# Kernel optimization log

Hardware: AMD Instinct MI355X
Metric: run time of the kernel (lower is better)

## Reference

```python
import jax, jax.numpy as jnp
import numpy as np

B, S, E, H = 2, 2048, 1024, 16
DK = E // H  # 64


def setup_inputs() -> dict:
    key = jax.random.key(0)
    ks = jax.random.split(key, 5)
    scale = 1.0 / np.sqrt(E)
    return {
        "x": jax.random.normal(ks[0], (B, S, E), dtype=jnp.float32),
        "Wq": jax.random.normal(ks[1], (E, E), dtype=jnp.float32) * scale,
        "Wk": jax.random.normal(ks[2], (E, E), dtype=jnp.float32) * scale,
        "Wv": jax.random.normal(ks[3], (E, E), dtype=jnp.float32) * scale,
        "Wo": jax.random.normal(ks[4], (E, E), dtype=jnp.float32) * scale,
    }


def reference(x, Wq, Wk, Wv, Wo):
    # Linear layers: y = x @ W.T (torch nn.Linear convention, bias=False)
    b, s, e = x.shape
    q = (x @ Wq.T).reshape(b, s, H, DK)  # (B,S,H,dk)
    k = (x @ Wk.T).reshape(b, s, H, DK)
    v = (x @ Wv.T).reshape(b, s, H, DK)
    # scores = Q K^T / sqrt(d_k)  -> (B,H,Sq,Sk)
    scores = jnp.einsum("bihd,bkhd->bhik", q, k) / jnp.sqrt(jnp.asarray(DK, x.dtype))
    p = jax.nn.softmax(scores, axis=-1)
    # dropout is identity in eval/deterministic mode
    attn = jnp.einsum("bhik,bkhd->bihd", p, v)  # (B,S,H,dk)
    concat = attn.reshape(b, s, e)
    return concat @ Wo.T
```

## Files before the change

### kernel.cpp

```cpp
#include <hip/hip_runtime.h>
#include <hip/hip_bf16.h>
#include <cstdint>
#include <cstddef>

typedef __bf16 bf16_t;
typedef __attribute__((ext_vector_type(8))) __bf16 bf16x8;
typedef __attribute__((ext_vector_type(4))) __bf16 bf16x4;
typedef __attribute__((ext_vector_type(4))) float f32x4;
typedef __attribute__((ext_vector_type(16))) float f32x16;
typedef uint32_t u32;
typedef __attribute__((ext_vector_type(4))) u32 u32x4;
typedef __attribute__((ext_vector_type(2))) u32 u32x2;

constexpr int B_ = 2, S_ = 2048, E_ = 1024, H_ = 16, DK_ = 64;

__device__ __forceinline__ void gl2lds16(const void* g, void* l) {
  __builtin_amdgcn_global_load_lds(
      (const __attribute__((address_space(1))) void*)g,
      (__attribute__((address_space(3))) void*)l, 16, 0, 0);
}

__device__ __forceinline__ float exp2_(float x) {
#if __has_builtin(__builtin_amdgcn_exp2f)
  return __builtin_amdgcn_exp2f(x);
#else
  return exp2f(x);
#endif
}

__device__ __forceinline__ u32 cvtpk(float lo, float hi) {
  u32 r;
  asm("v_cvt_pk_bf16_f32 %0, %1, %2" : "=v"(r) : "v"(lo), "v"(hi));
  return r;
}

__device__ __forceinline__ void pl32swap(u32& a, u32& b) {
#if __has_builtin(__builtin_amdgcn_permlane32_swap)
  const u32x2 r = __builtin_amdgcn_permlane32_swap(a, b, false, false);
  a = r[0]; b = r[1];
#else
  asm volatile("v_permlane32_swap_b32 %0, %1" : "+v"(a), "+v"(b));
#endif
}

__device__ __forceinline__ bf16x8 ldsfrag(const char* base, int row, int chunk) {
  return *reinterpret_cast<const bf16x8*>(base + row * 128 + (((chunk ^ (row & 7))) << 4));
}

__global__ __launch_bounds__(256) void f2bf_kernel(const float* __restrict__ in,
                                                   bf16_t* __restrict__ out, int n4) {
  int i = blockIdx.x * 256 + threadIdx.x;
  if (i >= n4) return;
  const float4 v = reinterpret_cast<const float4*>(in)[i];
  bf16x4 o;
  o[0] = (bf16_t)v.x; o[1] = (bf16_t)v.y; o[2] = (bf16_t)v.z; o[3] = (bf16_t)v.w;
  reinterpret_cast<bf16x4*>(out)[i] = o;
}

__global__ __launch_bounds__(256) void f2bf_w(const float* __restrict__ w0,
                                              const float* __restrict__ w1,
                                              const float* __restrict__ w2,
                                              const float* __restrict__ w3,
                                              bf16_t* __restrict__ out) {
  const int i = blockIdx.x * 256 + threadIdx.x;
  const int seg = i >> 18, off = i & 262143;
  const float* src = seg == 0 ? w0 : seg == 1 ? w1 : seg == 2 ? w2 : w3;
  const float4 v = reinterpret_cast<const float4*>(src)[off];
  bf16x4 o;
  o[0] = (bf16_t)v.x; o[1] = (bf16_t)v.y; o[2] = (bf16_t)v.z; o[3] = (bf16_t)v.w;
  reinterpret_cast<bf16x4*>(out)[i] = o;
}

__global__ __launch_bounds__(256) void gemm_qkv(const bf16_t* __restrict__ A,
                                                const bf16_t* __restrict__ Bt,
                                                bf16_t* __restrict__ Qo,
                                                bf16_t* __restrict__ Ko,
                                                bf16_t* __restrict__ Vto,
                                                int K, float qscale) {
  __shared__ bf16_t As[128 * 32];
  __shared__ bf16_t Bs[128 * 32];
  const int tid = threadIdx.x;
  const int w = tid >> 6, l = tid & 63;
  const int wr = w >> 1, wc = w & 1;
  const int tm = blockIdx.x * 128, tn = blockIdx.y * 128;
  f32x4 acc[4][4] = {};

  for (int k0 = 0; k0 < K; k0 += 32) {
#pragma unroll
    for (int i = 0; i < 2; ++i) {
      const int r = i * 64 + w * 16 + (l >> 2);
      const int c = k0 + (l & 3) * 8;
      gl2lds16(A + (size_t)(tm + r) * K + c, As + (i * 64 + w * 16) * 32);
      gl2lds16(Bt + (size_t)(tn + r) * K + c, Bs + (i * 64 + w * 16) * 32);
    }
    __syncthreads();

    bf16x8 af[4], bfr[4];
#pragma unroll
    for (int mi = 0; mi < 4; ++mi)
      af[mi] = *reinterpret_cast<const bf16x8*>(
          As + (wr * 64 + mi * 16 + (l & 15)) * 32 + (l >> 4) * 8);
#pragma unroll
    for (int ni = 0; ni < 4; ++ni)
      bfr[ni] = *reinterpret_cast<const bf16x8*>(
          Bs + (wc * 64 + ni * 16 + (l & 15)) * 32 + (l >> 4) * 8);
#pragma unroll
    for (int mi = 0; mi < 4; ++mi)
#pragma unroll
      for (int ni = 0; ni < 4; ++ni)
        acc[mi][ni] =
            __builtin_amdgcn_mfma_f32_16x16x32_bf16(af[mi], bfr[ni], acc[mi][ni], 0, 0, 0);
    __syncthreads();
  }

#pragma unroll
  for (int mi = 0; mi < 4; ++mi)
#pragma unroll
    for (int ni = 0; ni < 4; ++ni) {
      if (tn < 2048) {
        bf16_t* C = (tn < 1024) ? Qo : Ko;
        const float sc = (tn < 1024) ? qscale : 1.0f;
        const int colb = (tn < 1024) ? tn : tn - 1024;
#pragma unroll
        for (int r = 0; r < 4; ++r) {
          const int row = tm + wr * 64 + mi * 16 + (l >> 4) * 4 + r;
          const int col = colb + wc * 64 + ni * 16 + (l & 15);
          C[(size_t)row * 1024 + col] = (bf16_t)(acc[mi][ni][r] * sc);
        }
      } else {
        const int tok0 = tm + wr * 64 + mi * 16 + (l >> 4) * 4;
        const int feat = (tn - 2048) + wc * 64 + ni * 16 + (l & 15);
        const int b = tok0 >> 11, s = tok0 & 2047;
        bf16x4 o4;
#pragma unroll
        for (int r = 0; r < 4; ++r) o4[r] = (bf16_t)acc[mi][ni][r];
        *reinterpret_cast<bf16x4*>(Vto + (((size_t)(b * E_ + feat)) << 11) + s) = o4;
      }
    }
}

__global__ __launch_bounds__(256) void gemm_o(const bf16_t* __restrict__ A,
                                              const bf16_t* __restrict__ Bt,
                                              float* __restrict__ C,
                                              int M, int N, int K) {
  __shared__ bf16_t As[64 * 32];
  __shared__ bf16_t Bs[128 * 32];
  const int tid = threadIdx.x;
  const int w = tid >> 6, l = tid & 63;
  const int wr = w >> 1, wc = w & 1;
  const int tm = blockIdx.x * 64, tn = blockIdx.y * 128;
  f32x4 acc[2][4] = {};

  for (int k0 = 0; k0 < K; k0 += 32) {
    const int c = k0 + (l & 3) * 8;
    gl2lds16(A + (size_t)(tm + w * 16 + (l >> 2)) * K + c, As + (w * 16) * 32);
#pragma unroll
    for (int i = 0; i < 2; ++i)
      gl2lds16(Bt + (size_t)(tn + i * 64 + w * 16 + (l >> 2)) * K + c,
               Bs + (i * 64 + w * 16) * 32);
    __syncthreads();

    bf16x8 af[2], bfr[4];
#pragma unroll
    for (int mi = 0; mi < 2; ++mi)
      af[mi] = *reinterpret_cast<const bf16x8*>(
          As + (wr * 32 + mi * 16 + (l & 15)) * 32 + (l >> 4) * 8);
#pragma unroll
    for (int ni = 0; ni < 4; ++ni)
      bfr[ni] = *reinterpret_cast<const bf16x8*>(
          Bs + (wc * 64 + ni * 16 + (l & 15)) * 32 + (l >> 4) * 8);
#pragma unroll
    for (int mi = 0; mi < 2; ++mi)
#pragma unroll
      for (int ni = 0; ni < 4; ++ni)
        acc[mi][ni] =
            __builtin_amdgcn_mfma_f32_16x16x32_bf16(af[mi], bfr[ni], acc[mi][ni], 0, 0, 0);
    __syncthreads();
  }

#pragma unroll
  for (int mi = 0; mi < 2; ++mi)
#pragma unroll
    for (int ni = 0; ni < 4; ++ni)
#pragma unroll
      for (int r = 0; r < 4; ++r) {
        const int row = tm + wr * 32 + mi * 16 + (l >> 4) * 4 + r;
        const int col = tn + wc * 64 + ni * 16 + (l & 15);
        C[(size_t)row * N + col] = acc[mi][ni][r];
      }
}

template <int NSPL>
__global__ __launch_bounds__(256, 2) void attn_fwd(const bf16_t* __restrict__ Q,
                                                   const bf16_t* __restrict__ K,
                                                   const bf16_t* __restrict__ Vt,
                                                   bf16_t* __restrict__ O,
                                                   u32* __restrict__ Op,
                                                   float* __restrict__ lbuf) {
  __shared__ __align__(16) char smem[32768];
  const int tid = threadIdx.x;
  const int w = tid >> 6, l = tid & 63;
  const int hi = l >> 5, l31 = l & 31;
  const int nblk = 512 * NSPL;
  const int flat = blockIdx.x;
  const int wid = (flat & 7) * (nblk >> 3) + (flat >> 3);
  const int qb = wid & 15, bh = (wid >> 4) & 31;
  const int part = wid >> 9;
  const int q0 = qb * 128 + w * 32;
  const size_t hb = (size_t)(bh >> 4) * (S_ * E_) + (size_t)(bh & 15) * DK_;
  const bf16_t* const Qh = Q + hb;
  const bf16_t* const Kh = K + hb;
  const bf16_t* const Vth = Vt + (size_t)bh * (DK_ * S_);

  const int srow = l >> 3;
  const int schunk = (l & 7) ^ srow;

  bf16x8 ones;
  {
    u32x4 ow;
    ow[0] = 0x3F803F80u; ow[1] = 0x3F803F80u; ow[2] = 0x3F803F80u; ow[3] = 0x3F803F80u;
    ones = __builtin_bit_cast(bf16x8, ow);
  }

  bf16x8 qf[4];
#pragma unroll
  for (int df = 0; df < 4; ++df)
    qf[df] = *reinterpret_cast<const bf16x8*>(
        Qh + (size_t)(q0 + l31) * E_ + df * 16 + hi * 8);

  f32x16 oacc[2] = {};
  f32x16 lacc = {};
  const float mbase = 12.0f;

  auto stage = [&](int t, int buf) {
    const int t0 = t * 64;
#pragma unroll
    for (int i = 0; i < 2; ++i) {
      const int rg = w * 2 + i;
      const int row = rg * 8 + srow;
      gl2lds16(Kh + (size_t)(t0 + row) * E_ + schunk * 8,
               smem + buf * 8192 + rg * 1024);
      gl2lds16(Vth + (size_t)row * S_ + t0 + schunk * 8,
               smem + 16384 + buf * 8192 + rg * 1024);
    }
  };

  const int ntl = 32 / NSPL;
  const int tbeg = part * ntl;

  stage(tbeg, 0);
  stage(tbeg + 1, 1);

  for (int tt = 0; tt < ntl; ++tt) {
    const int cur = tt & 1;
    if (tt + 1 < ntl) asm volatile("s_waitcnt vmcnt(4)" ::: "memory");
    else              asm volatile("s_waitcnt vmcnt(0)" ::: "memory");
    __builtin_amdgcn_s_barrier();
    __builtin_amdgcn_sched_barrier(0);

    const char* const Kcur = smem + cur * 8192;
    const char* const Vcur = smem + 16384 + cur * 8192;

    f32x16 sacc[2] = {};
    __builtin_amdgcn_s_setprio(1);
#pragma unroll
    for (int kb = 0; kb < 2; ++kb)
#pragma unroll
      for (int df = 0; df < 4; ++df) {
        const bf16x8 kf = ldsfrag(Kcur, kb * 32 + l31, df * 2 + hi);
        sacc[kb] = __builtin_amdgcn_mfma_f32_32x32x16_bf16(kf, qf[df], sacc[kb], 0, 0, 0);
      }
    __builtin_amdgcn_s_setprio(0);

#pragma unroll
    for (int kb = 0; kb < 2; ++kb)
#pragma unroll
      for (int u = 0; u < 16; ++u)
        sacc[kb][u] = exp2_(sacc[kb][u] - mbase);

#pragma unroll
    for (int kf = 0; kf < 4; ++kf) {
      const int kb = kf >> 1, u0 = (kf & 1) * 8;
      u32 w0 = cvtpk(sacc[kb][u0 + 0], sacc[kb][u0 + 1]);
      u32 w1 = cvtpk(sacc[kb][u0 + 2], sacc[kb][u0 + 3]);
      u32 w2 = cvtpk(sacc[kb][u0 + 4], sacc[kb][u0 + 5]);
      u32 w3 = cvtpk(sacc[kb][u0 + 6], sacc[kb][u0 + 7]);
      pl32swap(w0, w2);
      pl32swap(w1, w3);
      u32x4 pw; pw[0] = w0; pw[1] = w1; pw[2] = w2; pw[3] = w3;
      const bf16x8 pa = __builtin_bit_cast(bf16x8, pw);
      __builtin_amdgcn_s_setprio(1);
#pragma unroll
      for (int dn = 0; dn < 2; ++dn) {
        const bf16x8 vf = ldsfrag(Vcur, dn * 32 + l31, kf * 2 + hi);
        oacc[dn] = __builtin_amdgcn_mfma_f32_32x32x16_bf16(pa, vf, oacc[dn], 0, 0, 0);
      }
      lacc = __builtin_amdgcn_mfma_f32_32x32x16_bf16(pa, ones, lacc, 0, 0, 0);
      __builtin_amdgcn_s_setprio(0);
    }

    if (tt + 2 < ntl) {
      __builtin_amdgcn_s_barrier();
      __builtin_amdgcn_sched_barrier(0);
      stage(tbeg + tt + 2, cur);
    }
  }

  if constexpr (NSPL > 1) {
    const int pb = part * 65536 + bh * S_;
#pragma unroll
    for (int u = 0; u < 16; ++u) {
      if (l31 == u) {
        const int q = q0 + (u & 3) + 8 * (u >> 2) + 4 * hi;
        lbuf[pb + q] = lacc[u];
      }
    }
    u32* const Oph = Op + (size_t)part * 2097152 + (size_t)(bh * S_) * 32 + l31;
#pragma unroll
    for (int u = 0; u < 16; ++u) {
      const int q = q0 + (u & 3) + 8 * (u >> 2) + 4 * hi;
      Oph[(size_t)q * 32] = cvtpk(oacc[0][u], oacc[1][u]);
    }
  } else {
#pragma unroll
    for (int u = 0; u < 16; ++u) {
      const float inv = 1.f / lacc[u];
      const int q = q0 + (u & 3) + 8 * (u >> 2) + 4 * hi;
      O[hb + (size_t)q * E_ + l31] = (bf16_t)(oacc[0][u] * inv);
      O[hb + (size_t)q * E_ + 32 + l31] = (bf16_t)(oacc[1][u] * inv);
    }
  }
}

__global__ __launch_bounds__(256) void attn_combine(const u32* __restrict__ Op,
                                                    const float* __restrict__ lbuf,
                                                    bf16_t* __restrict__ Ac) {
  const int idx = blockIdx.x * 256 + threadIdx.x;
  const int r = idx >> 5, c = idx & 31;
  const float lsum = lbuf[r] + lbuf[65536 + r];
  float o0 = 0.f, o1 = 0.f;
#pragma unroll
  for (int i = 0; i < 2; ++i) {
    const u32 p = Op[(size_t)i * 2097152 + (size_t)r * 32 + c];
    o0 += __builtin_bit_cast(float, p << 16);
    o1 += __builtin_bit_cast(float, p & 0xFFFF0000u);
  }
  const float inv = 1.f / lsum;
  const int q = r & 2047, bh = r >> 11;
  bf16_t* const base =
      Ac + (size_t)(bh >> 4) * (S_ * E_) + (size_t)q * E_ + (bh & 15) * DK_;
  base[c] = (bf16_t)(o0 * inv);
  base[c + 32] = (bf16_t)(o1 * inv);
}

extern "C" void kernel_launch(void* const* d_in, const int* in_sizes, int n_in,
                              void* d_out, int out_size, void* d_ws, size_t ws_size,
                              hipStream_t stream) {
  const float* x  = (const float*)d_in[0];
  const float* Wq = (const float*)d_in[1];
  const float* Wk = (const float*)d_in[2];
  const float* Wv = (const float*)d_in[3];
  const float* Wo = (const float*)d_in[4];
  float* out = (float*)d_out;

  bf16_t* xb  = (bf16_t*)d_ws;
  bf16_t* wqb = xb + 4194304;
  bf16_t* wob = wqb + 3145728;
  bf16_t* Qb  = wqb + 4194304;
  bf16_t* Kb  = Qb + 4194304;
  bf16_t* Vtb = Kb + 4194304;
  u32*    Opart = (u32*)(Vtb + 4194304);
  float*  lbuf  = (float*)d_ws;

  const bool split = ws_size >= 76546048ull;
  bf16_t* Ac = split ? Kb : xb;

  f2bf_kernel<<<4096, 256, 0, stream>>>(x, xb, 1048576);
  f2bf_w<<<4096, 256, 0, stream>>>(Wq, Wk, Wv, Wo, wqb);

  gemm_qkv<<<dim3(32, 24), 256, 0, stream>>>(xb, wqb, Qb, Kb, Vtb, 1024, 0.18033688f);

  if (split) {
    attn_fwd<2><<<1024, 256, 0, stream>>>(Qb, Kb, Vtb, nullptr, Opart, lbuf);
    attn_combine<<<8192, 256, 0, stream>>>(Opart, lbuf, Ac);
  } else {
    attn_fwd<1><<<512, 256, 0, stream>>>(Qb, Kb, Vtb, Ac, nullptr, nullptr);
  }

  gemm_o<<<dim3(64, 8), 256, 0, stream>>>(Ac, wob, out, 4096, 1024, 1024);
}
```

Measured before the change: 128.9 us.

## Fuse split-attention combine into output GEMM and merge conversion kernels

Removes the separate attn_combine kernel by having the output projection GEMM read the two partial attention outputs and row sums directly, normalize them, and pack bf16 A tiles into LDS. The two fp32-to-bf16 conversion kernels are also merged into one launch, and the exp bias is folded into the score accumulator's initial value. This saves two launches and a full intermediate write and read, but the A-tile load in the GEMM is now a synchronous register path with extra arithmetic instead of an asynchronous global-to-LDS copy.

```diff
diff --git a/kernel.cpp b/kernel.cpp
--- a/kernel.cpp
+++ b/kernel.cpp
@@ -47,24 +47,23 @@
   return *reinterpret_cast<const bf16x8*>(base + row * 128 + (((chunk ^ (row & 7))) << 4));
 }
 
-__global__ __launch_bounds__(256) void f2bf_kernel(const float* __restrict__ in,
-                                                   bf16_t* __restrict__ out, int n4) {
-  int i = blockIdx.x * 256 + threadIdx.x;
-  if (i >= n4) return;
-  const float4 v = reinterpret_cast<const float4*>(in)[i];
-  bf16x4 o;
-  o[0] = (bf16_t)v.x; o[1] = (bf16_t)v.y; o[2] = (bf16_t)v.z; o[3] = (bf16_t)v.w;
-  reinterpret_cast<bf16x4*>(out)[i] = o;
-}
-
-__global__ __launch_bounds__(256) void f2bf_w(const float* __restrict__ w0,
-                                              const float* __restrict__ w1,
-                                              const float* __restrict__ w2,
-                                              const float* __restrict__ w3,
-                                              bf16_t* __restrict__ out) {
+__global__ __launch_bounds__(256) void f2bf_all(const float* __restrict__ x,
+                                                const float* __restrict__ w0,
+                                                const float* __restrict__ w1,
+                                                const float* __restrict__ w2,
+                                                const float* __restrict__ w3,
+                                                bf16_t* __restrict__ out) {
   const int i = blockIdx.x * 256 + threadIdx.x;
-  const int seg = i >> 18, off = i & 262143;
-  const float* src = seg == 0 ? w0 : seg == 1 ? w1 : seg == 2 ? w2 : w3;
+  const float* src;
+  int off;
+  if (i < (1 << 20)) {
+    src = x; off = i;
+  } else {
+    const int j = i - (1 << 20);
+    const int s = j >> 18;
+    off = j & 262143;
+    src = s == 0 ? w0 : s == 1 ? w1 : s == 2 ? w2 : w3;
+  }
   const float4 v = reinterpret_cast<const float4*>(src)[off];
   bf16x4 o;
   o[0] = (bf16_t)v.x; o[1] = (bf16_t)v.y; o[2] = (bf16_t)v.z; o[3] = (bf16_t)v.w;
@@ -137,6 +136,88 @@
         *reinterpret_cast<bf16x4*>(Vto + (((size_t)(b * E_ + feat)) << 11) + s) = o4;
       }
     }
+}
+
+__global__ __launch_bounds__(256) void gemm_o_cmb(const u32* __restrict__ Op,
+                                                  const float* __restrict__ lbuf,
+                                                  const bf16_t* __restrict__ Bt,
+                                                  float* __restrict__ C) {
+  __shared__ bf16_t As[64 * 32];
+  __shared__ bf16_t Bs[128 * 32];
+  const int tid = threadIdx.x;
+  const int w = tid >> 6, l = tid & 63;
+  const int wr = w >> 1, wc = w & 1;
+  const int tm = blockIdx.x * 64, tn = blockIdx.y * 128;
+  f32x4 acc[2][4] = {};
+
+  const int arow = tm + (tid >> 2);
+  const int t4 = tid & 3;
+  const int b = arow >> 11, q = arow & 2047;
+
+  for (int k0 = 0; k0 < 1024; k0 += 32) {
+    {
+      const int head = k0 >> 6;
+      const int half = (k0 >> 5) & 1;
+      const size_t r = (size_t)((b << 4) + head) * 2048 + q;
+      const u32x4* const p0 = reinterpret_cast<const u32x4*>(Op + r * 32 + t4 * 8);
+      const u32x4* const p1 = reinterpret_cast<const u32x4*>(Op + 2097152 + r * 32 + t4 * 8);
+      const u32x4 a0 = p0[0], a1 = p0[1];
+      const u32x4 b0 = p1[0], b1 = p1[1];
+      const float inv = 1.f / (lbuf[r] + lbuf[65536 + r]);
+      float o[8];
+#pragma unroll
+      for (int j = 0; j < 4; ++j) {
+        const u32 u0 = a0[j], v0 = b0[j];
+        const u32 u1 = a1[j], v1 = b1[j];
+        o[j] = (half ? (__builtin_bit_cast(float, u0 & 0xFFFF0000u) +
+                        __builtin_bit_cast(float, v0 & 0xFFFF0000u))
+                     : (__builtin_bit_cast(float, u0 << 16) +
+                        __builtin_bit_cast(float, v0 << 16))) * inv;
+        o[j + 4] = (half ? (__builtin_bit_cast(float, u1 & 0xFFFF0000u) +
+                            __builtin_bit_cast(float, v1 & 0xFFFF0000u))
+                         : (__builtin_bit_cast(float, u1 << 16) +
+                            __builtin_bit_cast(float, v1 << 16))) * inv;
+      }
+      u32x4 pk;
+      pk[0] = cvtpk(o[0], o[1]); pk[1] = cvtpk(o[2], o[3]);
+      pk[2] = cvtpk(o[4], o[5]); pk[3] = cvtpk(o[6], o[7]);
+      *reinterpret_cast<u32x4*>(As + (tid >> 2) * 32 + t4 * 8) = pk;
+    }
+    const int c = k0 + (l & 3) * 8;
+#pragma unroll
+    for (int i = 0; i < 2; ++i)
+      gl2lds16(Bt + (size_t)(tn + i * 64 + w * 16 + (l >> 2)) * 1024 + c,
+               Bs + (i * 64 + w * 16) * 32);
+    __syncthreads();
+
+    bf16x8 af[2], bfr[4];
+#pragma unroll
+    for (int mi = 0; mi < 2; ++mi)
+      af[mi] = *reinterpret_cast<const bf16x8*>(
+          As + (wr * 32 + mi * 16 + (l & 15)) * 32 + (l >> 4) * 8);
+#pragma unroll
+    for (int ni = 0; ni < 4; ++ni)
+      bfr[ni] = *reinterpret_cast<const bf16x8*>(
+          Bs + (wc * 64 + ni * 16 + (l & 15)) * 32 + (l >> 4) * 8);
+#pragma unroll
+    for (int mi = 0; mi < 2; ++mi)
+#pragma unroll
+      for (int ni = 0; ni < 4; ++ni)
+        acc[mi][ni] =
+            __builtin_amdgcn_mfma_f32_16x16x32_bf16(af[mi], bfr[ni], acc[mi][ni], 0, 0, 0);
+    __syncthreads();
+  }
+
+#pragma unroll
+  for (int mi = 0; mi < 2; ++mi)
+#pragma unroll
+    for (int ni = 0; ni < 4; ++ni)
+#pragma unroll
+      for (int r = 0; r < 4; ++r) {
+        const int row = tm + wr * 32 + mi * 16 + (l >> 4) * 4 + r;
+        const int col = tn + wc * 64 + ni * 16 + (l & 15);
+        C[(size_t)row * 1024 + col] = acc[mi][ni][r];
+      }
 }
 
 __global__ __launch_bounds__(256) void gemm_o(const bf16_t* __restrict__ A,
@@ -230,7 +311,6 @@
 
   f32x16 oacc[2] = {};
   f32x16 lacc = {};
-  const float mbase = 12.0f;
 
   auto stage = [&](int t, int buf) {
     const int t0 = t * 64;
@@ -261,7 +341,11 @@
     const char* const Kcur = smem + cur * 8192;
     const char* const Vcur = smem + 16384 + cur * 8192;
 
-    f32x16 sacc[2] = {};
+    f32x16 sacc[2];
+#pragma unroll
+    for (int kb = 0; kb < 2; ++kb)
+#pragma unroll
+      for (int u = 0; u < 16; ++u) sacc[kb][u] = -12.0f;
     __builtin_amdgcn_s_setprio(1);
 #pragma unroll
     for (int kb = 0; kb < 2; ++kb)
@@ -276,7 +360,7 @@
     for (int kb = 0; kb < 2; ++kb)
 #pragma unroll
       for (int u = 0; u < 16; ++u)
-        sacc[kb][u] = exp2_(sacc[kb][u] - mbase);
+        sacc[kb][u] = exp2_(sacc[kb][u]);
 
 #pragma unroll
     for (int kf = 0; kf < 4; ++kf) {
@@ -332,27 +416,6 @@
   }
 }
 
-__global__ __launch_bounds__(256) void attn_combine(const u32* __restrict__ Op,
-                                                    const float* __restrict__ lbuf,
-                                                    bf16_t* __restrict__ Ac) {
-  const int idx = blockIdx.x * 256 + threadIdx.x;
-  const int r = idx >> 5, c = idx & 31;
-  const float lsum = lbuf[r] + lbuf[65536 + r];
-  float o0 = 0.f, o1 = 0.f;
-#pragma unroll
-  for (int i = 0; i < 2; ++i) {
-    const u32 p = Op[(size_t)i * 2097152 + (size_t)r * 32 + c];
-    o0 += __builtin_bit_cast(float, p << 16);
-    o1 += __builtin_bit_cast(float, p & 0xFFFF0000u);
-  }
-  const float inv = 1.f / lsum;
-  const int q = r & 2047, bh = r >> 11;
-  bf16_t* const base =
-      Ac + (size_t)(bh >> 4) * (S_ * E_) + (size_t)q * E_ + (bh & 15) * DK_;
-  base[c] = (bf16_t)(o0 * inv);
-  base[c + 32] = (bf16_t)(o1 * inv);
-}
-
 extern "C" void kernel_launch(void* const* d_in, const int* in_sizes, int n_in,
                               void* d_out, int out_size, void* d_ws, size_t ws_size,
                               hipStream_t stream) {
@@ -373,19 +436,17 @@
   float*  lbuf  = (float*)d_ws;
 
   const bool split = ws_size >= 76546048ull;
-  bf16_t* Ac = split ? Kb : xb;
-
-  f2bf_kernel<<<4096, 256, 0, stream>>>(x, xb, 1048576);
-  f2bf_w<<<4096, 256, 0, stream>>>(Wq, Wk, Wv, Wo, wqb);
+
+  f2bf_all<<<8192, 256, 0, stream>>>(x, Wq, Wk, Wv, Wo, xb);
 
   gemm_qkv<<<dim3(32, 24), 256, 0, stream>>>(xb, wqb, Qb, Kb, Vtb, 1024, 0.18033688f);
 
   if (split) {
     attn_fwd<2><<<1024, 256, 0, stream>>>(Qb, Kb, Vtb, nullptr, Opart, lbuf);
-    attn_combine<<<8192, 256, 0, stream>>>(Opart, lbuf, Ac);
+    gemm_o_cmb<<<dim3(64, 8), 256, 0, stream>>>(Opart, lbuf, wob, out);
   } else {
+    bf16_t* Ac = xb;
     attn_fwd<1><<<512, 256, 0, stream>>>(Qb, Kb, Vtb, Ac, nullptr, nullptr);
-  }
-
-  gemm_o<<<dim3(64, 8), 256, 0, stream>>>(Ac, wob, out, 4096, 1024, 1024);
-}
+    gemm_o<<<dim3(64, 8), 256, 0, stream>>>(Ac, wob, out, 4096, 1024, 1024);
+  }
+}
```

Result: no change. 128.8 us (-0.1%).

## Double-buffer GEMM LDS loads and merge fp32-to-bf16 conversion kernels

Applied to the files above, without the earlier changes.

Both projection GEMMs now use two LDS buffers with async global-to-LDS loads issued two k-steps ahead and explicit vmcnt waits, so memory latency can overlap the MFMA work. The two conversion kernels are merged into one launch, and K is made a compile-time constant. The attention kernel folds its softmax max-offset into the initial score accumulator, which removes a subtract per element. Doubling the LDS footprint may lower occupancy, and the hand-written vmcnt counts must match the number of issued loads.

```diff
diff --git a/kernel.cpp b/kernel.cpp
--- a/kernel.cpp
+++ b/kernel.cpp
@@ -47,24 +47,23 @@
   return *reinterpret_cast<const bf16x8*>(base + row * 128 + (((chunk ^ (row & 7))) << 4));
 }
 
-__global__ __launch_bounds__(256) void f2bf_kernel(const float* __restrict__ in,
-                                                   bf16_t* __restrict__ out, int n4) {
-  int i = blockIdx.x * 256 + threadIdx.x;
-  if (i >= n4) return;
-  const float4 v = reinterpret_cast<const float4*>(in)[i];
-  bf16x4 o;
-  o[0] = (bf16_t)v.x; o[1] = (bf16_t)v.y; o[2] = (bf16_t)v.z; o[3] = (bf16_t)v.w;
-  reinterpret_cast<bf16x4*>(out)[i] = o;
-}
-
-__global__ __launch_bounds__(256) void f2bf_w(const float* __restrict__ w0,
-                                              const float* __restrict__ w1,
-                                              const float* __restrict__ w2,
-                                              const float* __restrict__ w3,
-                                              bf16_t* __restrict__ out) {
+__global__ __launch_bounds__(256) void f2bf_all(const float* __restrict__ x,
+                                                const float* __restrict__ w0,
+                                                const float* __restrict__ w1,
+                                                const float* __restrict__ w2,
+                                                const float* __restrict__ w3,
+                                                bf16_t* __restrict__ out) {
   const int i = blockIdx.x * 256 + threadIdx.x;
-  const int seg = i >> 18, off = i & 262143;
-  const float* src = seg == 0 ? w0 : seg == 1 ? w1 : seg == 2 ? w2 : w3;
+  const float* src;
+  int off;
+  if (i < (1 << 20)) {
+    src = x; off = i;
+  } else {
+    const int j = i - (1 << 20);
+    const int s = j >> 18;
+    off = j & 262143;
+    src = s == 0 ? w0 : s == 1 ? w1 : s == 2 ? w2 : w3;
+  }
   const float4 v = reinterpret_cast<const float4*>(src)[off];
   bf16x4 o;
   o[0] = (bf16_t)v.x; o[1] = (bf16_t)v.y; o[2] = (bf16_t)v.z; o[3] = (bf16_t)v.w;
@@ -76,41 +75,57 @@
                                                 bf16_t* __restrict__ Qo,
                                                 bf16_t* __restrict__ Ko,
                                                 bf16_t* __restrict__ Vto,
-                                                int K, float qscale) {
-  __shared__ bf16_t As[128 * 32];
-  __shared__ bf16_t Bs[128 * 32];
+                                                float qscale) {
+  __shared__ bf16_t As[2][128 * 32];
+  __shared__ bf16_t Bs[2][128 * 32];
   const int tid = threadIdx.x;
   const int w = tid >> 6, l = tid & 63;
   const int wr = w >> 1, wc = w & 1;
   const int tm = blockIdx.x * 128, tn = blockIdx.y * 128;
+  constexpr int K = 1024, nk = K / 32;
   f32x4 acc[4][4] = {};
 
-  for (int k0 = 0; k0 < K; k0 += 32) {
+  auto stage = [&](int k0, int buf) {
 #pragma unroll
     for (int i = 0; i < 2; ++i) {
       const int r = i * 64 + w * 16 + (l >> 2);
       const int c = k0 + (l & 3) * 8;
-      gl2lds16(A + (size_t)(tm + r) * K + c, As + (i * 64 + w * 16) * 32);
-      gl2lds16(Bt + (size_t)(tn + r) * K + c, Bs + (i * 64 + w * 16) * 32);
-    }
-    __syncthreads();
+      gl2lds16(A + (size_t)(tm + r) * K + c, As[buf] + (i * 64 + w * 16) * 32);
+      gl2lds16(Bt + (size_t)(tn + r) * K + c, Bs[buf] + (i * 64 + w * 16) * 32);
+    }
+  };
+
+  stage(0, 0);
+  stage(32, 1);
+
+  for (int t = 0; t < nk; ++t) {
+    const int cur = t & 1;
+    if (t + 1 < nk) asm volatile("s_waitcnt vmcnt(4)" ::: "memory");
+    else            asm volatile("s_waitcnt vmcnt(0)" ::: "memory");
+    __builtin_amdgcn_s_barrier();
+    __builtin_amdgcn_sched_barrier(0);
 
     bf16x8 af[4], bfr[4];
 #pragma unroll
     for (int mi = 0; mi < 4; ++mi)
       af[mi] = *reinterpret_cast<const bf16x8*>(
-          As + (wr * 64 + mi * 16 + (l & 15)) * 32 + (l >> 4) * 8);
+          As[cur] + (wr * 64 + mi * 16 + (l & 15)) * 32 + (l >> 4) * 8);
 #pragma unroll
     for (int ni = 0; ni < 4; ++ni)
       bfr[ni] = *reinterpret_cast<const bf16x8*>(
-          Bs + (wc * 64 + ni * 16 + (l & 15)) * 32 + (l >> 4) * 8);
+          Bs[cur] + (wc * 64 + ni * 16 + (l & 15)) * 32 + (l >> 4) * 8);
 #pragma unroll
     for (int mi = 0; mi < 4; ++mi)
 #pragma unroll
       for (int ni = 0; ni < 4; ++ni)
         acc[mi][ni] =
             __builtin_amdgcn_mfma_f32_16x16x32_bf16(af[mi], bfr[ni], acc[mi][ni], 0, 0, 0);
-    __syncthreads();
+
+    if (t + 2 < nk) {
+      __builtin_amdgcn_s_barrier();
+      __builtin_amdgcn_sched_barrier(0);
+      stage((t + 2) * 32, cur);
+    }
   }
 
 #pragma unroll
@@ -141,41 +156,56 @@
 
 __global__ __launch_bounds__(256) void gemm_o(const bf16_t* __restrict__ A,
                                               const bf16_t* __restrict__ Bt,
-                                              float* __restrict__ C,
-                                              int M, int N, int K) {
-  __shared__ bf16_t As[64 * 32];
-  __shared__ bf16_t Bs[128 * 32];
+                                              float* __restrict__ C) {
+  __shared__ bf16_t As[2][64 * 32];
+  __shared__ bf16_t Bs[2][128 * 32];
   const int tid = threadIdx.x;
   const int w = tid >> 6, l = tid & 63;
   const int wr = w >> 1, wc = w & 1;
   const int tm = blockIdx.x * 64, tn = blockIdx.y * 128;
+  constexpr int K = 1024, nk = K / 32;
   f32x4 acc[2][4] = {};
 
-  for (int k0 = 0; k0 < K; k0 += 32) {
+  auto stage = [&](int k0, int buf) {
     const int c = k0 + (l & 3) * 8;
-    gl2lds16(A + (size_t)(tm + w * 16 + (l >> 2)) * K + c, As + (w * 16) * 32);
+    gl2lds16(A + (size_t)(tm + w * 16 + (l >> 2)) * K + c, As[buf] + (w * 16) * 32);
 #pragma unroll
     for (int i = 0; i < 2; ++i)
       gl2lds16(Bt + (size_t)(tn + i * 64 + w * 16 + (l >> 2)) * K + c,
-               Bs + (i * 64 + w * 16) * 32);
-    __syncthreads();
+               Bs[buf] + (i * 64 + w * 16) * 32);
+  };
+
+  stage(0, 0);
+  stage(32, 1);
+
+  for (int t = 0; t < nk; ++t) {
+    const int cur = t & 1;
+    if (t + 1 < nk) asm volatile("s_waitcnt vmcnt(3)" ::: "memory");
+    else            asm volatile("s_waitcnt vmcnt(0)" ::: "memory");
+    __builtin_amdgcn_s_barrier();
+    __builtin_amdgcn_sched_barrier(0);
 
     bf16x8 af[2], bfr[4];
 #pragma unroll
     for (int mi = 0; mi < 2; ++mi)
       af[mi] = *reinterpret_cast<const bf16x8*>(
-          As + (wr * 32 + mi * 16 + (l & 15)) * 32 + (l >> 4) * 8);
+          As[cur] + (wr * 32 + mi * 16 + (l & 15)) * 32 + (l >> 4) * 8);
 #pragma unroll
     for (int ni = 0; ni < 4; ++ni)
       bfr[ni] = *reinterpret_cast<const bf16x8*>(
-          Bs + (wc * 64 + ni * 16 + (l & 15)) * 32 + (l >> 4) * 8);
+          Bs[cur] + (wc * 64 + ni * 16 + (l & 15)) * 32 + (l >> 4) * 8);
 #pragma unroll
     for (int mi = 0; mi < 2; ++mi)
 #pragma unroll
       for (int ni = 0; ni < 4; ++ni)
         acc[mi][ni] =
             __builtin_amdgcn_mfma_f32_16x16x32_bf16(af[mi], bfr[ni], acc[mi][ni], 0, 0, 0);
-    __syncthreads();
+
+    if (t + 2 < nk) {
+      __builtin_amdgcn_s_barrier();
+      __builtin_amdgcn_sched_barrier(0);
+      stage((t + 2) * 32, cur);
+    }
   }
 
 #pragma unroll
@@ -186,7 +216,7 @@
       for (int r = 0; r < 4; ++r) {
         const int row = tm + wr * 32 + mi * 16 + (l >> 4) * 4 + r;
         const int col = tn + wc * 64 + ni * 16 + (l & 15);
-        C[(size_t)row * N + col] = acc[mi][ni][r];
+        C[(size_t)row * 1024 + col] = acc[mi][ni][r];
       }
 }
 
@@ -230,7 +260,6 @@
 
   f32x16 oacc[2] = {};
   f32x16 lacc = {};
-  const float mbase = 12.0f;
 
   auto stage = [&](int t, int buf) {
     const int t0 = t * 64;
@@ -261,7 +290,11 @@
     const char* const Kcur = smem + cur * 8192;
     const char* const Vcur = smem + 16384 + cur * 8192;
 
-    f32x16 sacc[2] = {};
+    f32x16 sacc[2];
+#pragma unroll
+    for (int kb = 0; kb < 2; ++kb)
+#pragma unroll
+      for (int u = 0; u < 16; ++u) sacc[kb][u] = -12.0f;
     __builtin_amdgcn_s_setprio(1);
 #pragma unroll
     for (int kb = 0; kb < 2; ++kb)
@@ -276,7 +309,7 @@
     for (int kb = 0; kb < 2; ++kb)
 #pragma unroll
       for (int u = 0; u < 16; ++u)
-        sacc[kb][u] = exp2_(sacc[kb][u] - mbase);
+        sacc[kb][u] = exp2_(sacc[kb][u]);
 
 #pragma unroll
     for (int kf = 0; kf < 4; ++kf) {
@@ -373,19 +406,19 @@
   float*  lbuf  = (float*)d_ws;
 
   const bool split = ws_size >= 76546048ull;
-  bf16_t* Ac = split ? Kb : xb;
-
-  f2bf_kernel<<<4096, 256, 0, stream>>>(x, xb, 1048576);
-  f2bf_w<<<4096, 256, 0, stream>>>(Wq, Wk, Wv, Wo, wqb);
-
-  gemm_qkv<<<dim3(32, 24), 256, 0, stream>>>(xb, wqb, Qb, Kb, Vtb, 1024, 0.18033688f);
+
+  f2bf_all<<<8192, 256, 0, stream>>>(x, Wq, Wk, Wv, Wo, xb);
+
+  gemm_qkv<<<dim3(32, 24), 256, 0, stream>>>(xb, wqb, Qb, Kb, Vtb, 0.18033688f);
 
   if (split) {
+    bf16_t* Ac = Kb;
     attn_fwd<2><<<1024, 256, 0, stream>>>(Qb, Kb, Vtb, nullptr, Opart, lbuf);
     attn_combine<<<8192, 256, 0, stream>>>(Opart, lbuf, Ac);
+    gemm_o<<<dim3(64, 8), 256, 0, stream>>>(Ac, wob, out);
   } else {
+    bf16_t* Ac = xb;
     attn_fwd<1><<<512, 256, 0, stream>>>(Qb, Kb, Vtb, Ac, nullptr, nullptr);
-  }
-
-  gemm_o<<<dim3(64, 8), 256, 0, stream>>>(Ac, wob, out, 4096, 1024, 1024);
-}
+    gemm_o<<<dim3(64, 8), 256, 0, stream>>>(Ac, wob, out);
+  }
+}
```

After: 117.1 us. -9.2%, faster.
